# Kernel optimization log

Measured on AMD Instinct MI355X. Metric: run time of the kernel, lower is better.

The kernel has to match this reference:

```python
import jax, jax.numpy as jnp
import numpy as np

BN_EPS = 1e-3

def hard_sigmoid(x):
    # Keras-style hard sigmoid used by LSTMHardSigmoid recurrent gates
    return jnp.clip(0.2 * x + 0.5, 0.0, 1.0)

def lstm_dir(x, w_ih, w_hh, b, reverse):
    # x: [B,S,D]; w_ih: [4H,D]; w_hh: [4H,H]; b: [4H] (b_ih+b_hh combined)
    H = w_hh.shape[1]
    xg = jnp.einsum('bsd,gd->bsg', x, w_ih) + b  # precompute input projection [B,S,4H]
    if reverse:
        xg = xg[:, ::-1]
    def step(carry, xg_t):
        h, c = carry
        g = xg_t + h @ w_hh.T
        i, f, gg, o = jnp.split(g, 4, axis=-1)  # PyTorch gate order i,f,g,o
        i = hard_sigmoid(i); f = hard_sigmoid(f)
        gg = jnp.tanh(gg); o = hard_sigmoid(o)
        c = f * c + i * gg
        h = o * jnp.tanh(c)
        return (h, c), h
    B = x.shape[0]
    h0 = jnp.zeros((B, H), x.dtype)
    _, hs = jax.lax.scan(step, (h0, h0), jnp.swapaxes(xg, 0, 1))
    hs = jnp.swapaxes(hs, 0, 1)  # [B,S,H]
    if reverse:
        hs = hs[:, ::-1]
    return hs

def bilstm(x, wf_ih, wf_hh, bf, wb_ih, wb_hh, bb):
    fwd = lstm_dir(x, wf_ih, wf_hh, bf, False)
    bwd = lstm_dir(x, wb_ih, wb_hh, bb, True)
    return jnp.concatenate([fwd, bwd], axis=-1)

def setup_inputs() -> dict:
    key = jax.random.key(0)
    ks = iter(jax.random.split(key, 64))
    d = {}
    d['x'] = jax.random.randint(next(ks), (64, 512), 0, 149)
    s = 0.08
    d['emb'] = jax.random.normal(next(ks), (149, 288), jnp.float32) * s
    layers = [(288, 288), (576, 144), (288, 96)]
    for l, (din, h) in enumerate(layers):
        for dr in ('f', 'b'):
            d[f'w_ih_{l}{dr}'] = jax.random.normal(next(ks), (4 * h, din), jnp.float32) * s
            d[f'w_hh_{l}{dr}'] = jax.random.normal(next(ks), (4 * h, h), jnp.float32) * s
            d[f'b_{l}{dr}'] = jax.random.normal(next(ks), (4 * h,), jnp.float32) * s
    d['bn_gamma'] = jnp.ones((576,), jnp.float32)
    d['bn_beta'] = jnp.zeros((576,), jnp.float32)
    d['bn_mean'] = jax.random.normal(next(ks), (576,), jnp.float32) * 0.1
    d['bn_var'] = jax.random.uniform(next(ks), (576,), jnp.float32, 0.5, 1.5)
    d['dense_w'] = jax.random.normal(next(ks), (28, 192), jnp.float32) * s
    d['dense_b'] = jnp.zeros((28,), jnp.float32)
    return d

def reference(x, emb,
              w_ih_0f, w_hh_0f, b_0f, w_ih_0b, w_hh_0b, b_0b,
              w_ih_1f, w_hh_1f, b_1f, w_ih_1b, w_hh_1b, b_1b,
              w_ih_2f, w_hh_2f, b_2f, w_ih_2b, w_hh_2b, b_2b,
              bn_gamma, bn_beta, bn_mean, bn_var, dense_w, dense_b):
    h = emb[x]  # [B,S,288]
    h = bilstm(h, w_ih_0f, w_hh_0f, b_0f, w_ih_0b, w_hh_0b, b_0b)  # [B,S,576]
    # BatchNorm1d in eval mode over channel dim
    h = (h - bn_mean) * jax.lax.rsqrt(bn_var + BN_EPS) * bn_gamma + bn_beta
    h = bilstm(h, w_ih_1f, w_hh_1f, b_1f, w_ih_1b, w_hh_1b, b_1b)  # [B,S,288]
    h = bilstm(h, w_ih_2f, w_hh_2f, b_2f, w_ih_2b, w_hh_2b, b_2b)  # [B,S,192]
    logits = jnp.einsum('bsd,od->bso', h, dense_w) + dense_b
    return jax.nn.softmax(logits, axis=-1)
```

## Files before the change

### kernel.cpp

```cpp
#include <hip/hip_runtime.h>
#include <stdint.h>

typedef __attribute__((ext_vector_type(8))) short short8v;
typedef __attribute__((ext_vector_type(4))) short short4v;
typedef __attribute__((ext_vector_type(4))) float float4v;

__device__ __forceinline__ float bf2f(short u) {
  union { unsigned int i; float f; } v;
  v.i = ((unsigned int)(unsigned short)u) << 16;
  return v.f;
}
__device__ __forceinline__ short f2bf(float f) {
  union { float f; unsigned int i; } v; v.f = f;
  unsigned int x = v.i;
  unsigned int r = (x + 0x7fffu + ((x >> 16) & 1u)) >> 16;
  return (short)r;
}
__device__ __forceinline__ float hsigf(float x) {
  return fminf(fmaxf(fmaf(x, 0.2f, 0.5f), 0.0f), 1.0f);
}
__device__ __forceinline__ float tanhf_fast(float x) {
  float e = __expf(2.0f * x);
  return 1.0f - __fdividef(2.0f, e + 1.0f);
}
__device__ __forceinline__ void gload_lds16(const void* g, void* l) {
  __builtin_amdgcn_global_load_lds((const __attribute__((address_space(1))) void*)g,
                                   (__attribute__((address_space(3))) void*)l, 16, 0, 0);
}
__device__ __forceinline__ short8v gload16_cc(const short* p) {
  short8v r;
  asm volatile("global_load_dwordx4 %0, %1, off sc0 sc1" : "=v"(r) : "v"(p));
  return r;
}
__device__ __forceinline__ void pina(short8v& v) { asm volatile("" : "+a"(v)); }
__device__ __forceinline__ void mfma_bA(float4v& d, short8v a, short8v b) {
  asm volatile("v_mfma_f32_16x16x32_bf16 %0, %1, %2, %0"
               : "+v"(d) : "v"(a), "a"(b));
}

__global__ __launch_bounds__(256)
void prep_misc(const float* __restrict__ wih0f, const float* __restrict__ wih0b,
               const float* __restrict__ whh0f, const float* __restrict__ whh0b,
               const float* __restrict__ wih2f, const float* __restrict__ wih2b,
               const float* __restrict__ whh2f, const float* __restrict__ whh2b,
               const float* __restrict__ whh1f, const float* __restrict__ whh1b,
               const float* __restrict__ b0f, const float* __restrict__ b0b,
               const float* __restrict__ b2f, const float* __restrict__ b2b,
               short* __restrict__ WG0, short* __restrict__ WG2,
               short* __restrict__ WHH0, short* __restrict__ WHH1, short* __restrict__ WHH2,
               float* __restrict__ B0, float* __restrict__ B2) {
  int i = blockIdx.x * 256 + threadIdx.x;
  if (i < 663552) { WG0[i] = f2bf(i < 331776 ? wih0f[i] : wih0b[i - 331776]); return; }
  i -= 663552;
  if (i < 221184) { WG2[i] = f2bf(i < 110592 ? wih2f[i] : wih2b[i - 110592]); return; }
  i -= 221184;
  if (i < 663552) { WHH0[i] = f2bf(i < 331776 ? whh0f[i] : whh0b[i - 331776]); return; }
  i -= 663552;
  if (i < 184320) {
    int n = i / 160, k = i - n * 160;
    float v = 0.0f;
    if (k < 144) v = (n < 576) ? whh1f[n * 144 + k] : whh1b[(n - 576) * 144 + k];
    WHH1[i] = f2bf(v); return;
  }
  i -= 184320;
  if (i < 73728) { WHH2[i] = f2bf(i < 36864 ? whh2f[i] : whh2b[i - 36864]); return; }
  i -= 73728;
  if (i < 2304) { B0[i] = (i < 1152) ? b0f[i] : b0b[i - 1152]; return; }
  i -= 2304;
  if (i < 768) { B2[i] = (i < 384) ? b2f[i] : b2b[i - 384]; return; }
}

__global__ __launch_bounds__(64)
void prep_bn(const float* __restrict__ w1f, const float* __restrict__ w1b,
             const float* __restrict__ bf1, const float* __restrict__ bb1,
             const float* __restrict__ gamma, const float* __restrict__ beta,
             const float* __restrict__ mean, const float* __restrict__ var,
             short* __restrict__ WG1, float* __restrict__ B1) {
  int n = blockIdx.x;
  int lane = threadIdx.x;
  const float* wrow = (n < 576) ? (w1f + (long)n * 576) : (w1b + (long)(n - 576) * 576);
  float bsrc = (n < 576) ? bf1[n] : bb1[n - 576];
  float part = 0.0f;
  for (int k = lane; k < 576; k += 64) {
    float sc = gamma[k] * rsqrtf(var[k] + 1e-3f);
    float off = beta[k] - mean[k] * sc;
    float w = wrow[k];
    WG1[(long)n * 576 + k] = f2bf(w * sc);
    part += w * off;
  }
#pragma unroll
  for (int m = 32; m >= 1; m >>= 1) part += __shfl_xor(part, m, 64);
  if (lane == 0) B1[n] = bsrc + part;
}

__global__ __launch_bounds__(256)
void embed_k(const int* __restrict__ x, const float* __restrict__ emb, short* __restrict__ A0) {
  int p0 = blockIdx.x * 16;
  for (int j = threadIdx.x; j < 16 * 72; j += 256) {
    int p = p0 + j / 72;
    int cc = j - (j / 72) * 72;
    int idx = x[p];
    float4v v = *(const float4v*)(emb + (long)idx * 288 + cc * 4);
    short4v s;
    s[0] = f2bf(v[0]); s[1] = f2bf(v[1]); s[2] = f2bf(v[2]); s[3] = f2bf(v[3]);
    *(short4v*)(A0 + (long)p * 288 + cc * 4) = s;
  }
}

__global__ __launch_bounds__(256)
void gemm_xg(const short* __restrict__ A, const short* __restrict__ W,
             const float* __restrict__ bias, short* __restrict__ C,
             int M, int N, int K, int H4, int H) {
  __shared__ short As[128 * 32];
  __shared__ short Bs[128 * 32];
  const int nbn = N >> 7;
  const int bm = blockIdx.x / nbn;
  const int bn = blockIdx.x - bm * nbn;
  const long m0 = (long)bm << 7;
  const int n0 = bn << 7;
  const int tid = threadIdx.x;
  const int lane = tid & 63, wv = tid >> 6;
  const int wr = wv >> 1, wc = wv & 1;
  const int l15 = lane & 15, l4 = lane >> 4;

  float4v acc[4][4];
#pragma unroll
  for (int j = 0; j < 4; ++j) {
    float bvj = bias[n0 + wc * 64 + j * 16 + l15];
#pragma unroll
    for (int i = 0; i < 4; ++i) acc[i][j] = float4v{bvj, bvj, bvj, bvj};
  }

  for (int kt = 0; kt < K; kt += 32) {
#pragma unroll
    for (int c = 0; c < 2; ++c) {
      int ci = wv * 128 + c * 64 + lane;
      int row = ci >> 2, slot = ci & 3;
      int k8 = slot ^ (row & 3);
      gload_lds16(A + (m0 + row) * K + kt + k8 * 8, &As[ci * 8]);
      gload_lds16(W + (long)(n0 + row) * K + kt + k8 * 8, &Bs[ci * 8]);
    }
    __syncthreads();
    short8v af[4], bf[4];
#pragma unroll
    for (int i = 0; i < 4; ++i) {
      int row = wr * 64 + i * 16 + l15;
      af[i] = *(const short8v*)&As[row * 32 + ((l4 ^ (row & 3)) * 8)];
    }
#pragma unroll
    for (int j = 0; j < 4; ++j) {
      int row = wc * 64 + j * 16 + l15;
      bf[j] = *(const short8v*)&Bs[row * 32 + ((l4 ^ (row & 3)) * 8)];
    }
#pragma unroll
    for (int i = 0; i < 4; ++i)
#pragma unroll
      for (int j = 0; j < 4; ++j)
        acc[i][j] = __builtin_amdgcn_mfma_f32_16x16x32_bf16(af[i], bf[j], acc[i][j], 0, 0, 0);
    __syncthreads();
  }

#pragma unroll
  for (int j = 0; j < 4; ++j) {
    int n = n0 + wc * 64 + j * 16 + l15;
    int dir = n / H4;
    int rem = n - dir * H4;
    int q = rem / H;
    int u = rem - q * H;
    long np = (long)dir * H4 + u * 4 + q;
#pragma unroll
    for (int i = 0; i < 4; ++i) {
#pragma unroll
      for (int r = 0; r < 4; ++r) {
        long row = m0 + wr * 64 + i * 16 + l4 * 4 + r;
        C[row * N + np] = f2bf(acc[i][j][r]);
      }
    }
  }
}

template<int H, int NK, int NU>
__global__ __launch_bounds__(256)
__attribute__((amdgpu_waves_per_eu(1, 1)))
void lstm_recX(const short* __restrict__ xg, int ldxg,
               const short* __restrict__ whh,
               short* __restrict__ out, int ldo,
               int* __restrict__ fl) {
  constexpr int KPAD = NK * 32;
  const int dir = blockIdx.x & 1;
  const int us = blockIdx.x >> 1;
  const int tid = threadIdx.x;
  const int lane = tid & 63;
  const int mt = tid >> 6;
  const int l15 = lane & 15, l4 = lane >> 4;
  int* fl_d = fl + dir * 512 * 128;
  const short* whh_d = whh + (long)dir * (4 * H) * KPAD;
  const int xoff = dir * 4 * H;
  const int ooff = dir * H;
  const int u = us * 16 + l15;

  short8v bw[4][NK];
#pragma unroll
  for (int q = 0; q < 4; ++q)
#pragma unroll
    for (int kk = 0; kk < NK; ++kk) {
      bw[q][kk] = *(const short8v*)(whh_d + (long)(q * H + u) * KPAD + kk * 32 + l4 * 8);
      pina(bw[q][kk]);
    }

  float cst[4] = {0.0f, 0.0f, 0.0f, 0.0f};
  const int flidx = (lane < NU) ? lane : 0;

  for (int t = 0; t < 512; ++t) {
    const int te = dir ? (511 - t) : t;

    short4v x4[4];
#pragma unroll
    for (int r = 0; r < 4; ++r) {
      const long b_ = mt * 16 + l4 * 4 + r;
      x4[r] = *(const short4v*)(xg + (b_ * 512 + te) * ldxg + xoff + u * 4);
    }

    float4v a0 = {0, 0, 0, 0}, a1 = {0, 0, 0, 0}, a2 = {0, 0, 0, 0}, a3 = {0, 0, 0, 0};
    if (t > 0) {
      const int tp = dir ? (te + 1) : (te - 1);
      int* fb = fl_d + (t - 1) * 128 + flidx * 4 + mt;
      while (!__all(__hip_atomic_load(fb, __ATOMIC_RELAXED, __HIP_MEMORY_SCOPE_AGENT) != 0)) {}
      __builtin_amdgcn_sched_barrier(0);
      const short* hbase = out + ((long)(mt * 16 + l15) * 512 + tp) * ldo + ooff + l4 * 8;
      short8v a[NK];
#pragma unroll
      for (int kk = 0; kk < NK; ++kk) a[kk] = gload16_cc(hbase + kk * 32);
      asm volatile("s_waitcnt vmcnt(0)" ::: "memory");
      __builtin_amdgcn_sched_barrier(0);
      asm volatile("s_nop 1" :::);
#pragma unroll
      for (int kk = 0; kk < NK; ++kk) {
        mfma_bA(a0, a[kk], bw[0][kk]);
        mfma_bA(a1, a[kk], bw[1][kk]);
        mfma_bA(a2, a[kk], bw[2][kk]);
        mfma_bA(a3, a[kk], bw[3][kk]);
      }
      asm volatile("s_nop 7\n\ts_nop 7" :::);
    }

#pragma unroll
    for (int r = 0; r < 4; ++r) {
      const long b_ = mt * 16 + l4 * 4 + r;
      const long orow = (b_ * 512 + te) * ldo;
      float gi_ = a0[r] + bf2f(x4[r][0]);
      float gf_ = a1[r] + bf2f(x4[r][1]);
      float gg_ = a2[r] + bf2f(x4[r][2]);
      float go_ = a3[r] + bf2f(x4[r][3]);
      float iv = hsigf(gi_), fv = hsigf(gf_), gv = tanhf_fast(gg_), ov = hsigf(go_);
      float cn = fv * cst[r] + iv * gv;
      cst[r] = cn;
      __hip_atomic_store(out + orow + ooff + u, f2bf(ov * tanhf_fast(cn)),
                         __ATOMIC_RELAXED, __HIP_MEMORY_SCOPE_AGENT);
    }

    asm volatile("s_waitcnt vmcnt(0)" ::: "memory");
    if (lane == 0)
      __hip_atomic_store(fl_d + t * 128 + us * 4 + mt, 1,
                         __ATOMIC_RELAXED, __HIP_MEMORY_SCOPE_AGENT);
  }
}

template<int H, int NK, int NG, int NGW>
__global__ __launch_bounds__(256)
__attribute__((amdgpu_waves_per_eu(1, 1)))
void lstm_loc(const short* __restrict__ xg, int ldxg,
              const short* __restrict__ whh,
              short* __restrict__ out, int ldo) {
  constexpr int KPAD = NK * 32;
  constexpr int HP = KPAD + 8;
  __shared__ __align__(16) short hbuf[2][16][HP];
  const int dir = blockIdx.x & 1;
  const int bg = blockIdx.x >> 1;
  const int b0 = bg * 16;
  const int tid = threadIdx.x;
  const int lane = tid & 63, wv = tid >> 6;
  const int l15 = lane & 15, l4 = lane >> 4;
  const short* whh_d = whh + (long)dir * (4 * H) * KPAD;
  const int xoff = dir * 4 * H;
  const int ooff = dir * H;

  int u[NGW];
#pragma unroll
  for (int j = 0; j < NGW; ++j) {
    int g = wv + 4 * j; if (g > NG - 1) g = NG - 1;
    u[j] = g * 16 + l15;
  }

  {
    short* hf = &hbuf[0][0][0];
    for (int i = tid; i < 2 * 16 * HP; i += 256) hf[i] = 0;
  }

  short8v bw[NGW][4][NK];
#pragma unroll
  for (int j = 0; j < NGW; ++j)
#pragma unroll
    for (int q = 0; q < 4; ++q)
#pragma unroll
      for (int kk = 0; kk < NK; ++kk) {
        bw[j][q][kk] = *(const short8v*)(whh_d + (long)(q * H + u[j]) * KPAD + kk * 32 + l4 * 8);
        pina(bw[j][q][kk]);
      }

  float cst[NGW][4];
#pragma unroll
  for (int j = 0; j < NGW; ++j)
#pragma unroll
    for (int r = 0; r < 4; ++r) cst[j][r] = 0.0f;

  const int te0 = dir ? 511 : 0;
  short4v xc[NGW][4], xn[NGW][4];
#pragma unroll
  for (int j = 0; j < NGW; ++j)
#pragma unroll
    for (int r = 0; r < 4; ++r)
      xc[j][r] = *(const short4v*)(xg + ((long)(b0 + l4 * 4 + r) * 512 + te0) * ldxg + xoff + u[j] * 4);

  asm volatile("s_waitcnt lgkmcnt(0)" ::: "memory");
  __builtin_amdgcn_s_barrier();
  asm volatile("" ::: "memory");

  for (int t = 0; t < 512; ++t) {
    const int te = dir ? (511 - t) : t;
    const int cur = t & 1;

    float4v A[NGW][4];
#pragma unroll
    for (int j = 0; j < NGW; ++j)
#pragma unroll
      for (int q = 0; q < 4; ++q) A[j][q] = float4v{0, 0, 0, 0};

    if (t > 0) {
      short8v a[NK];
#pragma unroll
      for (int kk = 0; kk < NK; ++kk)
        a[kk] = *(const short8v*)&hbuf[cur ^ 1][l15][kk * 32 + l4 * 8];
      asm volatile("s_nop 1" :::);
#pragma unroll
      for (int j = 0; j < NGW; ++j)
#pragma unroll
        for (int kk = 0; kk < NK; ++kk) {
          mfma_bA(A[j][0], a[kk], bw[j][0][kk]);
          mfma_bA(A[j][1], a[kk], bw[j][1][kk]);
          mfma_bA(A[j][2], a[kk], bw[j][2][kk]);
          mfma_bA(A[j][3], a[kk], bw[j][3][kk]);
        }
      asm volatile("s_nop 7\n\ts_nop 7" :::);
    }

    if (t < 511) {
      const int ten = dir ? (te - 1) : (te + 1);
#pragma unroll
      for (int j = 0; j < NGW; ++j)
#pragma unroll
        for (int r = 0; r < 4; ++r)
          xn[j][r] = *(const short4v*)(xg + ((long)(b0 + l4 * 4 + r) * 512 + ten) * ldxg + xoff + u[j] * 4);
    }

#pragma unroll
    for (int j = 0; j < NGW; ++j)
#pragma unroll
      for (int r = 0; r < 4; ++r) {
        const long b_ = b0 + l4 * 4 + r;
        const long orow = (b_ * 512 + te) * ldo;
        float gi_ = A[j][0][r] + bf2f(xc[j][r][0]);
        float gf_ = A[j][1][r] + bf2f(xc[j][r][1]);
        float gg_ = A[j][2][r] + bf2f(xc[j][r][2]);
        float go_ = A[j][3][r] + bf2f(xc[j][r][3]);
        float iv = hsigf(gi_), fv = hsigf(gf_), gv = tanhf_fast(gg_), ov = hsigf(go_);
        float cn = fv * cst[j][r] + iv * gv;
        cst[j][r] = cn;
        short hb = f2bf(ov * tanhf_fast(cn));
        hbuf[cur][l4 * 4 + r][u[j]] = hb;
        out[orow + ooff + u[j]] = hb;
      }

#pragma unroll
    for (int j = 0; j < NGW; ++j)
#pragma unroll
      for (int r = 0; r < 4; ++r) xc[j][r] = xn[j][r];

    asm volatile("s_waitcnt lgkmcnt(0)" ::: "memory");
    __builtin_amdgcn_s_barrier();
    asm volatile("" ::: "memory");
    __builtin_amdgcn_sched_barrier(0);
  }
}

__global__ __launch_bounds__(256)
void dense_sm(const short* __restrict__ h, const float* __restrict__ w,
              const float* __restrict__ b, float* __restrict__ out) {
  __shared__ float wl[28 * 192];
  for (int i = threadIdx.x; i < 28 * 192; i += 256) wl[i] = w[i];
  __syncthreads();
  long m = (long)blockIdx.x * 256 + threadIdx.x;
  const short* hr = h + m * 192;
  float acc[28];
#pragma unroll
  for (int o = 0; o < 28; ++o) acc[o] = b[o];
  for (int cch = 0; cch < 24; ++cch) {
    short8v hv = *(const short8v*)(hr + cch * 8);
    float hf[8];
#pragma unroll
    for (int j = 0; j < 8; ++j) hf[j] = bf2f(hv[j]);
#pragma unroll
    for (int o = 0; o < 28; ++o) {
      const float* wp = &wl[o * 192 + cch * 8];
#pragma unroll
      for (int j = 0; j < 8; ++j) acc[o] = fmaf(hf[j], wp[j], acc[o]);
    }
  }
  float mx = acc[0];
#pragma unroll
  for (int o = 1; o < 28; ++o) mx = fmaxf(mx, acc[o]);
  float s = 0.0f;
#pragma unroll
  for (int o = 0; o < 28; ++o) { float e = __expf(acc[o] - mx); acc[o] = e; s += e; }
  float r = __fdividef(1.0f, s);
#pragma unroll
  for (int o = 0; o < 28; ++o) out[m * 28 + o] = acc[o] * r;
}

extern "C" void kernel_launch(void* const* d_in, const int* in_sizes, int n_in,
                              void* d_out, int out_size, void* d_ws, size_t ws_size,
                              hipStream_t stream) {
  const int*   x     = (const int*)d_in[0];
  const float* emb   = (const float*)d_in[1];
  const float* wih0f = (const float*)d_in[2];
  const float* whh0f = (const float*)d_in[3];
  const float* b0f   = (const float*)d_in[4];
  const float* wih0b = (const float*)d_in[5];
  const float* whh0b = (const float*)d_in[6];
  const float* b0b   = (const float*)d_in[7];
  const float* wih1f = (const float*)d_in[8];
  const float* whh1f = (const float*)d_in[9];
  const float* b1f   = (const float*)d_in[10];
  const float* wih1b = (const float*)d_in[11];
  const float* whh1b = (const float*)d_in[12];
  const float* b1b   = (const float*)d_in[13];
  const float* wih2f = (const float*)d_in[14];
  const float* whh2f = (const float*)d_in[15];
  const float* b2f   = (const float*)d_in[16];
  const float* wih2b = (const float*)d_in[17];
  const float* whh2b = (const float*)d_in[18];
  const float* b2b   = (const float*)d_in[19];
  const float* gamma = (const float*)d_in[20];
  const float* beta  = (const float*)d_in[21];
  const float* mean  = (const float*)d_in[22];
  const float* var   = (const float*)d_in[23];
  const float* dw    = (const float*)d_in[24];
  const float* db    = (const float*)d_in[25];

  char* ws = (char*)d_ws;
  size_t off = 0;
  auto alloc = [&](size_t bytes) -> void* {
    void* p = (void*)(ws + off);
    off += (bytes + 255) & ~(size_t)255;
    return p;
  };
  short* A0   = (short*)alloc(32768L * 288 * 2);
  short* XG   = (short*)alloc(32768L * 2304 * 2);
  short* OUT0 = (short*)alloc(32768L * 576 * 2);
  short* OUT1 = (short*)alloc(32768L * 288 * 2);
  short* OUT2 = (short*)alloc(32768L * 192 * 2);
  short* WG0  = (short*)alloc(2304L * 288 * 2);
  short* WG1  = (short*)alloc(1152L * 576 * 2);
  short* WG2  = (short*)alloc(768L * 288 * 2);
  short* WHH0 = (short*)alloc(2304L * 288 * 2);
  short* WHH1 = (short*)alloc(1152L * 160 * 2);
  short* WHH2 = (short*)alloc(768L * 96 * 2);
  float* B0   = (float*)alloc(2304 * 4);
  float* B1   = (float*)alloc(1152 * 4);
  float* B2   = (float*)alloc(768 * 4);
  int* FL     = (int*)alloc(2 * 512 * 128 * 4);
  if (off > ws_size) return;

  hipMemsetAsync(FL, 0, 2 * 512 * 128 * 4, stream);

  prep_misc<<<dim3(7068), dim3(256), 0, stream>>>(
      wih0f, wih0b, whh0f, whh0b, wih2f, wih2b, whh2f, whh2b, whh1f, whh1b,
      b0f, b0b, b2f, b2b, WG0, WG2, WHH0, WHH1, WHH2, B0, B2);
  prep_bn<<<dim3(1152), dim3(64), 0, stream>>>(
      wih1f, wih1b, b1f, b1b, gamma, beta, mean, var, WG1, B1);
  embed_k<<<dim3(2048), dim3(256), 0, stream>>>(x, emb, A0);

  gemm_xg<<<dim3(256 * 18), dim3(256), 0, stream>>>(A0, WG0, B0, XG, 32768, 2304, 288, 1152, 288);
  hipLaunchKernelGGL(HIP_KERNEL_NAME(lstm_recX<288, 9, 18>), dim3(36), dim3(256), 0, stream,
                     XG, 2304, WHH0, OUT0, 576, FL);
  gemm_xg<<<dim3(256 * 9), dim3(256), 0, stream>>>(OUT0, WG1, B1, XG, 32768, 1152, 576, 576, 144);
  hipLaunchKernelGGL(HIP_KERNEL_NAME(lstm_loc<144, 5, 9, 3>), dim3(8), dim3(256), 0, stream,
                     XG, 1152, WHH1, OUT1, 288);
  gemm_xg<<<dim3(256 * 6), dim3(256), 0, stream>>>(OUT1, WG2, B2, XG, 32768, 768, 288, 384, 96);
  hipLaunchKernelGGL(HIP_KERNEL_NAME(lstm_loc<96, 3, 6, 2>), dim3(8), dim3(256), 0, stream,
                     XG, 768, WHH2, OUT2, 192);
  dense_sm<<<dim3(128), dim3(256), 0, stream>>>(OUT2, dw, db, (float*)d_out);
}
```

Before: 4.404 ms.

## Replace flag-based step sync with tagged hidden-state words in layer-0 recurrence

```diff
diff --git a/kernel.cpp b/kernel.cpp
--- a/kernel.cpp
+++ b/kernel.cpp
@@ -4,6 +4,7 @@
 typedef __attribute__((ext_vector_type(8))) short short8v;
 typedef __attribute__((ext_vector_type(4))) short short4v;
 typedef __attribute__((ext_vector_type(4))) float float4v;
+typedef __attribute__((ext_vector_type(4))) unsigned int uint4v;
 
 __device__ __forceinline__ float bf2f(short u) {
   union { unsigned int i; float f; } v;
@@ -27,8 +28,8 @@
   __builtin_amdgcn_global_load_lds((const __attribute__((address_space(1))) void*)g,
                                    (__attribute__((address_space(3))) void*)l, 16, 0, 0);
 }
-__device__ __forceinline__ short8v gload16_cc(const short* p) {
-  short8v r;
+__device__ __forceinline__ uint4v gload16_cu(const unsigned int* p) {
+  uint4v r;
   asm volatile("global_load_dwordx4 %0, %1, off sc0 sc1" : "=v"(r) : "v"(p));
   return r;
 }
@@ -179,13 +180,13 @@
   }
 }
 
-template<int H, int NK, int NU>
+template<int H, int NK>
 __global__ __launch_bounds__(256)
 __attribute__((amdgpu_waves_per_eu(1, 1)))
-void lstm_recX(const short* __restrict__ xg, int ldxg,
+void lstm_recT(const short* __restrict__ xg, int ldxg,
                const short* __restrict__ whh,
                short* __restrict__ out, int ldo,
-               int* __restrict__ fl) {
+               unsigned int* __restrict__ comm, int ldc) {
   constexpr int KPAD = NK * 32;
   const int dir = blockIdx.x & 1;
   const int us = blockIdx.x >> 1;
@@ -193,7 +194,6 @@
   const int lane = tid & 63;
   const int mt = tid >> 6;
   const int l15 = lane & 15, l4 = lane >> 4;
-  int* fl_d = fl + dir * 512 * 128;
   const short* whh_d = whh + (long)dir * (4 * H) * KPAD;
   const int xoff = dir * 4 * H;
   const int ooff = dir * H;
@@ -209,7 +209,6 @@
     }
 
   float cst[4] = {0.0f, 0.0f, 0.0f, 0.0f};
-  const int flidx = (lane < NU) ? lane : 0;
 
   for (int t = 0; t < 512; ++t) {
     const int te = dir ? (511 - t) : t;
@@ -224,15 +223,40 @@
     float4v a0 = {0, 0, 0, 0}, a1 = {0, 0, 0, 0}, a2 = {0, 0, 0, 0}, a3 = {0, 0, 0, 0};
     if (t > 0) {
       const int tp = dir ? (te + 1) : (te - 1);
-      int* fb = fl_d + (t - 1) * 128 + flidx * 4 + mt;
-      while (!__all(__hip_atomic_load(fb, __ATOMIC_RELAXED, __HIP_MEMORY_SCOPE_AGENT) != 0)) {}
+      const unsigned int tagw = (unsigned int)(tp + 1) << 16;
+      const unsigned int* cbase =
+          comm + ((long)(mt * 16 + l15) * 4 + (tp & 3)) * ldc + ooff + l4 * 8;
+      uint4v w[NK][2];
+      while (true) {
+#pragma unroll
+        for (int kk = 0; kk < NK; ++kk) {
+          w[kk][0] = gload16_cu(cbase + kk * 32);
+          w[kk][1] = gload16_cu(cbase + kk * 32 + 4);
+        }
+        asm volatile("s_waitcnt vmcnt(0)" ::: "memory");
+        __builtin_amdgcn_sched_barrier(0);
+        unsigned int bad = 0;
+#pragma unroll
+        for (int kk = 0; kk < NK; ++kk)
+#pragma unroll
+          for (int c = 0; c < 2; ++c)
+#pragma unroll
+            for (int j = 0; j < 4; ++j)
+              bad |= (w[kk][c][j] ^ tagw) & 0xFFFF0000u;
+        if (__all(bad == 0)) break;
+        __builtin_amdgcn_s_sleep(1);
+      }
       __builtin_amdgcn_sched_barrier(0);
-      const short* hbase = out + ((long)(mt * 16 + l15) * 512 + tp) * ldo + ooff + l4 * 8;
       short8v a[NK];
 #pragma unroll
-      for (int kk = 0; kk < NK; ++kk) a[kk] = gload16_cc(hbase + kk * 32);
-      asm volatile("s_waitcnt vmcnt(0)" ::: "memory");
-      __builtin_amdgcn_sched_barrier(0);
+      for (int kk = 0; kk < NK; ++kk) {
+        union { unsigned int q[4]; short8v s; } pk;
+        pk.q[0] = (w[kk][0][0] & 0xFFFFu) | (w[kk][0][1] << 16);
+        pk.q[1] = (w[kk][0][2] & 0xFFFFu) | (w[kk][0][3] << 16);
+        pk.q[2] = (w[kk][1][0] & 0xFFFFu) | (w[kk][1][1] << 16);
+        pk.q[3] = (w[kk][1][2] & 0xFFFFu) | (w[kk][1][3] << 16);
+        a[kk] = pk.s;
+      }
       asm volatile("s_nop 1" :::);
 #pragma unroll
       for (int kk = 0; kk < NK; ++kk) {
@@ -244,10 +268,10 @@
       asm volatile("s_nop 7\n\ts_nop 7" :::);
     }
 
+    const unsigned int mytag = (unsigned int)(te + 1) << 16;
 #pragma unroll
     for (int r = 0; r < 4; ++r) {
       const long b_ = mt * 16 + l4 * 4 + r;
-      const long orow = (b_ * 512 + te) * ldo;
       float gi_ = a0[r] + bf2f(x4[r][0]);
       float gf_ = a1[r] + bf2f(x4[r][1]);
       float gg_ = a2[r] + bf2f(x4[r][2]);
@@ -255,14 +279,12 @@
       float iv = hsigf(gi_), fv = hsigf(gf_), gv = tanhf_fast(gg_), ov = hsigf(go_);
       float cn = fv * cst[r] + iv * gv;
       cst[r] = cn;
-      __hip_atomic_store(out + orow + ooff + u, f2bf(ov * tanhf_fast(cn)),
+      short hb = f2bf(ov * tanhf_fast(cn));
+      out[(b_ * 512 + te) * ldo + ooff + u] = hb;
+      __hip_atomic_store(comm + (b_ * 4 + (te & 3)) * ldc + ooff + u,
+                         mytag | (unsigned int)(unsigned short)hb,
                          __ATOMIC_RELAXED, __HIP_MEMORY_SCOPE_AGENT);
     }
-
-    asm volatile("s_waitcnt vmcnt(0)" ::: "memory");
-    if (lane == 0)
-      __hip_atomic_store(fl_d + t * 128 + us * 4 + mt, 1,
-                         __ATOMIC_RELAXED, __HIP_MEMORY_SCOPE_AGENT);
   }
 }
 
@@ -478,10 +500,10 @@
   float* B0   = (float*)alloc(2304 * 4);
   float* B1   = (float*)alloc(1152 * 4);
   float* B2   = (float*)alloc(768 * 4);
-  int* FL     = (int*)alloc(2 * 512 * 128 * 4);
+  unsigned int* COMM = (unsigned int*)alloc(64L * 4 * 576 * 4);
   if (off > ws_size) return;
 
-  hipMemsetAsync(FL, 0, 2 * 512 * 128 * 4, stream);
+  hipMemsetAsync(COMM, 0, 64L * 4 * 576 * 4, stream);
 
   prep_misc<<<dim3(7068), dim3(256), 0, stream>>>(
       wih0f, wih0b, whh0f, whh0b, wih2f, wih2b, whh2f, whh2b, whh1f, whh1b,
@@ -491,8 +513,8 @@
   embed_k<<<dim3(2048), dim3(256), 0, stream>>>(x, emb, A0);
 
   gemm_xg<<<dim3(256 * 18), dim3(256), 0, stream>>>(A0, WG0, B0, XG, 32768, 2304, 288, 1152, 288);
-  hipLaunchKernelGGL(HIP_KERNEL_NAME(lstm_recX<288, 9, 18>), dim3(36), dim3(256), 0, stream,
-                     XG, 2304, WHH0, OUT0, 576, FL);
+  hipLaunchKernelGGL(HIP_KERNEL_NAME(lstm_recT<288, 9>), dim3(36), dim3(256), 0, stream,
+                     XG, 2304, WHH0, OUT0, 576, COMM, 576);
   gemm_xg<<<dim3(256 * 9), dim3(256), 0, stream>>>(OUT0, WG1, B1, XG, 32768, 1152, 576, 576, 144);
   hipLaunchKernelGGL(HIP_KERNEL_NAME(lstm_loc<144, 5, 9, 3>), dim3(8), dim3(256), 0, stream,
                      XG, 1152, WHH1, OUT1, 288);
```

Measured after the change: 4.999 ms. 1.14x slower.
